# Optimization experiments

Hardware: AMD Instinct MI355X
Metric: run time of the kernel (lower is better)

Reference implementation:

```python
import math
import jax, jax.numpy as jnp
import numpy as np

K = 4          # beats_per_bar
POS_DIM = 32   # fourier pos-embed dim


def setup_inputs() -> dict:
    key = jax.random.key(0)
    k1, k2, k3 = jax.random.split(key, 3)
    B, M, D = 8, 8192, 1024
    beat_emb = jax.random.normal(k1, (B, M, D), dtype=jnp.float32)
    W = jax.random.normal(k2, (D, D + POS_DIM), dtype=jnp.float32) * 0.02  # nn.Linear weight [out, in]
    b = jax.random.normal(k3, (D,), dtype=jnp.float32) * 0.02
    return {"beat_emb": beat_emb, "W": W, "b": b}


def _fourier_features(pos, dim):
    # pos: [Mb] in [0,1] -> [Mb, dim] (dim even, so no zero-pad branch needed)
    half = dim // 2
    freqs = jnp.exp(jnp.linspace(0.0, math.log(1000.0), half)).astype(pos.dtype)
    ang = pos[:, None] * freqs  # [Mb, half]
    return jnp.concatenate([jnp.sin(ang), jnp.cos(ang)], axis=-1)


def reference(beat_emb, W, b):
    B, M, D = beat_emb.shape
    Mb = (M + K - 1) // K
    pad = Mb * K - M
    x = jnp.pad(beat_emb, ((0, 0), (0, pad), (0, 0))) if pad else beat_emb
    # fused segment mean: [B, Mb, K, D] -> sum -> divide by actual segment length
    sums = x.reshape(B, Mb, K, D).sum(axis=2)
    counts = jnp.minimum(K, M - jnp.arange(Mb) * K).astype(beat_emb.dtype)  # [Mb]
    out = sums / counts[None, :, None]  # [B, Mb, D]
    # fourier positional features on normalized bar index (same for every batch row)
    idx = jnp.arange(Mb, dtype=beat_emb.dtype)
    pos = jnp.clip(idx / max(1, Mb - 1), 0.0, 1.0)
    ff = _fourier_features(pos, POS_DIM)                     # [Mb, POS_DIM]
    ff = jnp.broadcast_to(ff[None], (B, Mb, POS_DIM))
    h = jnp.concatenate([out, ff], axis=-1)                  # [B, Mb, D+POS_DIM]
    return jnp.einsum('bmi,oi->bmo', h, W) + b               # Linear: x @ W.T + b
```

## Files before the change

### kernel.cpp

```cpp
#include <hip/hip_runtime.h>
#include <math.h>
#include <stdint.h>
#include <stddef.h>

typedef short bf16x8 __attribute__((ext_vector_type(8)));
typedef short bf16x4 __attribute__((ext_vector_type(4)));
typedef float f32x4  __attribute__((ext_vector_type(4)));

#define BATCH   8
#define D       1024
#define POSD    32
#define WIN     1056
#define MBARS   2048
#define MROWS   16384
#define NOUT    1024

__device__ __forceinline__ short f2bf(float f) {
    unsigned u = __builtin_bit_cast(unsigned, f);
    u += 0x7fffu + ((u >> 16) & 1u);
    return (short)(u >> 16);
}

__device__ __forceinline__ void async_load16(const short* g, short* l) {
    __builtin_amdgcn_global_load_lds((__attribute__((address_space(1))) void*)g,
                                     (__attribute__((address_space(3))) void*)l,
                                     16, 0, 0);
}

__global__ __launch_bounds__(256) void prep3(const float* __restrict__ x,
                                             const float* __restrict__ W,
                                             const float* __restrict__ bias,
                                             short* __restrict__ h,
                                             short* __restrict__ Wb,
                                             float* __restrict__ FFW) {
    const int t   = threadIdx.x;
    const int bid = blockIdx.x;
    if (bid < MROWS) {
        const float4* src = (const float4*)(x + (size_t)bid * 4096);
        float4 s0 = src[t], s1 = src[t + 256], s2 = src[t + 512], s3 = src[t + 768];
        bf16x4 o = { f2bf((s0.x + s1.x + s2.x + s3.x) * 0.25f),
                     f2bf((s0.y + s1.y + s2.y + s3.y) * 0.25f),
                     f2bf((s0.z + s1.z + s2.z + s3.z) * 0.25f),
                     f2bf((s0.w + s1.w + s2.w + s3.w) * 0.25f) };
        *(bf16x4*)(h + (size_t)bid * D + t * 4) = o;
    } else if (bid < MROWS + NOUT) {
        const int rw = bid - MROWS;
        float4 v = ((const float4*)(W + (size_t)rw * WIN))[t];
        bf16x4 o = { f2bf(v.x), f2bf(v.y), f2bf(v.z), f2bf(v.w) };
        *(bf16x4*)(Wb + (size_t)rw * D + t * 4) = o;
    } else {
        const int mb0 = (bid - MROWS - NOUT) * 8;
        __shared__ float ff[8][32];
        if (t < 32) {
            float fr = expf((float)(t & 15) * (6.907755278982137f / 15.0f));
#pragma unroll
            for (int e = 0; e < 8; ++e) {
                float pos = (float)(mb0 + e) * (1.0f / (float)(MBARS - 1));
                float ang = pos * fr;
                ff[e][t] = (t < 16) ? sinf(ang) : cosf(ang);
            }
        }
        __syncthreads();
#pragma unroll
        for (int u = 0; u < 4; ++u) {
            const int n = t + u * 256;
            const float* wp = W + (size_t)n * WIN + D;
            float4 wv[8];
#pragma unroll
            for (int blk = 0; blk < 8; ++blk) wv[blk] = ((const float4*)wp)[blk];
            const float bn = bias[n];
#pragma unroll
            for (int e = 0; e < 8; ++e) {
                float s = bn;
#pragma unroll
                for (int blk = 0; blk < 8; ++blk) {
                    s += ff[e][blk * 4 + 0] * wv[blk].x + ff[e][blk * 4 + 1] * wv[blk].y
                       + ff[e][blk * 4 + 2] * wv[blk].z + ff[e][blk * 4 + 3] * wv[blk].w;
                }
                FFW[(size_t)(mb0 + e) * NOUT + n] = s;
            }
        }
    }
}

__global__ __launch_bounds__(256) void gemm_bt(const short* __restrict__ A,
                                               const short* __restrict__ B,
                                               const float* __restrict__ FFW,
                                               float* __restrict__ C) {
    __shared__ short As[128 * 64];
    __shared__ short Bs[128 * 64];

    const int tid  = threadIdx.x;
    const int wave = tid >> 6;
    const int lane = tid & 63;
    const int wrow = wave >> 1;
    const int wcol = wave & 1;

    const int m0 = blockIdx.x * 128;
    const int n0 = blockIdx.y * 128;

    const int r8   = tid >> 3;
    const int soct = (tid & 7) ^ (r8 & 7);
    const short* ag = A + (size_t)(m0 + r8) * D + soct * 8;
    const short* bg = B + (size_t)(n0 + r8) * D + soct * 8;
    short* al = As + wave * 512;
    short* bl = Bs + wave * 512;

    const int r  = lane & 15;
    const int q  = lane >> 4;
    const int rx = r & 7;
    const short* afr = As + (wrow * 64 + r) * 64;
    const short* bfr = Bs + (wcol * 64 + r) * 64;
    const int sl0 = ((q    ) ^ rx) * 8;
    const int sl1 = ((4 + q) ^ rx) * 8;

    f32x4 acc[4][4] = {};

    for (int k0 = 0; k0 < D; k0 += 64) {
        __syncthreads();
#pragma unroll
        for (int i = 0; i < 4; ++i) {
            async_load16(ag + k0 + (size_t)i * 32 * D, al + i * 2048);
            async_load16(bg + k0 + (size_t)i * 32 * D, bl + i * 2048);
        }
        __syncthreads();

#pragma unroll
        for (int s = 0; s < 2; ++s) {
            const int sl = s ? sl1 : sl0;
            bf16x8 a[4], b[4];
#pragma unroll
            for (int i = 0; i < 4; ++i) {
                a[i] = *(const bf16x8*)(afr + i * 1024 + sl);
                b[i] = *(const bf16x8*)(bfr + i * 1024 + sl);
            }
#pragma unroll
            for (int i = 0; i < 4; ++i)
#pragma unroll
                for (int j = 0; j < 4; ++j)
                    acc[i][j] = __builtin_amdgcn_mfma_f32_16x16x32_bf16(a[i], b[j], acc[i][j], 0, 0, 0);
        }
    }

    const int rr0 = m0 + wrow * 64 + (q << 2);
    const int c0  = n0 + wcol * 64 + r;
#pragma unroll
    for (int i = 0; i < 4; ++i)
#pragma unroll
        for (int rg = 0; rg < 4; ++rg) {
            const int row = rr0 + i * 16 + rg;
            const float* fw = FFW + (size_t)(row & (MBARS - 1)) * NOUT + c0;
            float* cp = C + (size_t)row * NOUT + c0;
#pragma unroll
            for (int j = 0; j < 4; ++j)
                cp[j * 16] = acc[i][j][rg] + fw[j * 16];
        }
}

extern "C" void kernel_launch(void* const* d_in, const int* in_sizes, int n_in,
                              void* d_out, int out_size, void* d_ws, size_t ws_size,
                              hipStream_t stream) {
    const float* x    = (const float*)d_in[0];
    const float* W    = (const float*)d_in[1];
    const float* bias = (const float*)d_in[2];
    float* out = (float*)d_out;

    short* Wb  = (short*)d_ws;
    float* FFW = (float*)((char*)d_ws + (size_t)NOUT * D * sizeof(short));
    short* h   = (short*)((char*)FFW + (size_t)MBARS * NOUT * sizeof(float));

    prep3  <<<dim3(MROWS + NOUT + MBARS / 8), dim3(256), 0, stream>>>(x, W, bias, h, Wb, FFW);
    gemm_bt<<<dim3(MROWS / 128, NOUT / 128), dim3(256), 0, stream>>>(h, Wb, FFW, out);
}
```

Measured before the change: 434.5 us.

## Double-buffer A tiles in LDS and stream B fragments straight from global

The GEMM now double-buffers the A tile in LDS: the next k-slice is prefetched with async global-to-LDS loads and gated by explicit vmcnt waits and raw barriers. B fragments skip LDS and are loaded directly from global memory into registers for each MFMA step. The launch bounds also ask for three blocks per CU. The aim is to overlap A transfers with compute and to halve LDS traffic and footprint. The cost is uncoalesced, repeated global loads of B in the inner loop, whose latency is not prefetched and may stall the MFMAs.

```diff
diff --git a/kernel.cpp b/kernel.cpp
--- a/kernel.cpp
+++ b/kernel.cpp
@@ -25,6 +25,12 @@
     __builtin_amdgcn_global_load_lds((__attribute__((address_space(1))) void*)g,
                                      (__attribute__((address_space(3))) void*)l,
                                      16, 0, 0);
+}
+
+__device__ __forceinline__ void bar() {
+    asm volatile("" ::: "memory");
+    __builtin_amdgcn_s_barrier();
+    asm volatile("" ::: "memory");
 }
 
 __global__ __launch_bounds__(256) void prep3(const float* __restrict__ x,
@@ -83,12 +89,11 @@
     }
 }
 
-__global__ __launch_bounds__(256) void gemm_bt(const short* __restrict__ A,
-                                               const short* __restrict__ B,
-                                               const float* __restrict__ FFW,
-                                               float* __restrict__ C) {
-    __shared__ short As[128 * 64];
-    __shared__ short Bs[128 * 64];
+__global__ __launch_bounds__(256, 3) void gemm_bt(const short* __restrict__ A,
+                                                  const short* __restrict__ B,
+                                                  const float* __restrict__ FFW,
+                                                  float* __restrict__ C) {
+    __shared__ short As[2 * 128 * 64];
 
     const int tid  = threadIdx.x;
     const int wave = tid >> 6;
@@ -102,44 +107,52 @@
     const int r8   = tid >> 3;
     const int soct = (tid & 7) ^ (r8 & 7);
     const short* ag = A + (size_t)(m0 + r8) * D + soct * 8;
-    const short* bg = B + (size_t)(n0 + r8) * D + soct * 8;
-    short* al = As + wave * 512;
-    short* bl = Bs + wave * 512;
+    const int    al = wave * 512;
 
     const int r  = lane & 15;
     const int q  = lane >> 4;
     const int rx = r & 7;
-    const short* afr = As + (wrow * 64 + r) * 64;
-    const short* bfr = Bs + (wcol * 64 + r) * 64;
+    const int ab = (wrow * 64 + r) * 64;
     const int sl0 = ((q    ) ^ rx) * 8;
     const int sl1 = ((4 + q) ^ rx) * 8;
 
+    const short* bgl = B + (size_t)(n0 + wcol * 64 + r) * D + q * 8;
+
     f32x4 acc[4][4] = {};
 
-    for (int k0 = 0; k0 < D; k0 += 64) {
-        __syncthreads();
 #pragma unroll
-        for (int i = 0; i < 4; ++i) {
-            async_load16(ag + k0 + (size_t)i * 32 * D, al + i * 2048);
-            async_load16(bg + k0 + (size_t)i * 32 * D, bl + i * 2048);
+    for (int i = 0; i < 4; ++i)
+        async_load16(ag + (size_t)i * 32 * D, As + al + i * 2048);
+
+    for (int k0 = 0; k0 < 16; ++k0) {
+        if (k0 < 15) {
+            const short* agk = ag + (k0 + 1) * 64;
+            short* nb = As + (((k0 + 1) & 1) << 13) + al;
+#pragma unroll
+            for (int i = 0; i < 4; ++i)
+                async_load16(agk + (size_t)i * 32 * D, nb + i * 2048);
         }
-        __syncthreads();
+        if (k0 < 15) asm volatile("s_waitcnt vmcnt(4)" ::: "memory");
+        else         asm volatile("s_waitcnt vmcnt(0)" ::: "memory");
+        bar();
 
+        const short* ap = As + ((k0 & 1) << 13) + ab;
+        const int kc = k0 * 64;
 #pragma unroll
         for (int s = 0; s < 2; ++s) {
             const int sl = s ? sl1 : sl0;
             bf16x8 a[4], b[4];
 #pragma unroll
-            for (int i = 0; i < 4; ++i) {
-                a[i] = *(const bf16x8*)(afr + i * 1024 + sl);
-                b[i] = *(const bf16x8*)(bfr + i * 1024 + sl);
-            }
+            for (int i = 0; i < 4; ++i) a[i] = *(const bf16x8*)(ap + i * 1024 + sl);
+#pragma unroll
+            for (int j = 0; j < 4; ++j) b[j] = *(const bf16x8*)(bgl + (size_t)j * 16 * D + kc + s * 32);
 #pragma unroll
             for (int i = 0; i < 4; ++i)
 #pragma unroll
                 for (int j = 0; j < 4; ++j)
                     acc[i][j] = __builtin_amdgcn_mfma_f32_16x16x32_bf16(a[i], b[j], acc[i][j], 0, 0, 0);
         }
+        bar();
     }
 
     const int rr0 = m0 + wrow * 64 + (q << 2);
```

Measured after the change: 461.0 us. +6.1%, slower.
